# Performance work log

Hardware: AMD Instinct MI355X
Metric: run time of the kernel (lower is better)

Reference implementation:

```python
import jax, jax.numpy as jnp
import numpy as np
from jax import lax

STRIDE = 16
SCALES = (8.0, 16.0, 32.0)
RATIOS = (0.5, 1.0, 2.0)
PRE_NMS = 6000
POST_NMS = 300
NMS_THRESH = 0.7
MIN_SIZE = 16.0
DN = ('NCHW', 'OIHW', 'NCHW')


def _base_anchors():
    # 9 base anchors centered at (STRIDE/2, STRIDE/2), (ymin,xmin,ymax,xmax)
    c = STRIDE / 2.0
    rows = []
    for r in RATIOS:
        for s in SCALES:
            h = STRIDE * s * np.sqrt(r)
            w = STRIDE * s * np.sqrt(1.0 / r)
            rows.append([c - h / 2, c - w / 2, c + h / 2, c + w / 2])
    return jnp.asarray(np.array(rows, np.float32))


def _all_anchors(wdim, hdim):
    # shift base anchors over the (w, h) feature grid, matching permute(0,2,3,1) flatten order
    sy = jnp.arange(wdim, dtype=jnp.float32) * STRIDE
    sx = jnp.arange(hdim, dtype=jnp.float32) * STRIDE
    yy, xx = jnp.meshgrid(sy, sx, indexing='ij')
    shifts = jnp.stack([yy, xx, yy, xx], axis=-1).reshape(-1, 4)  # [w*h, 4]
    return (shifts[:, None, :] + _base_anchors()[None, :, :]).reshape(-1, 4)  # [w*h*9, 4]


def _conv(x, W, b, pad):
    y = lax.conv_general_dilated(x, W, (1, 1), pad, dimension_numbers=DN)
    return y + b[None, :, None, None]


def _nms_fixed(boxes, keep):
    # sequential greedy NMS over score-sorted boxes; returns POST_NMS boxes (zero padded)
    y1, x1, y2, x2 = boxes[:, 0], boxes[:, 1], boxes[:, 2], boxes[:, 3]
    areas = (y2 - y1) * (x2 - x1)
    N = boxes.shape[0]
    idxs = jnp.arange(N)

    def body(i, keep):
        yy1 = jnp.maximum(y1[i], y1)
        xx1 = jnp.maximum(x1[i], x1)
        yy2 = jnp.minimum(y2[i], y2)
        xx2 = jnp.minimum(x2[i], x2)
        inter = jnp.maximum(yy2 - yy1, 0.0) * jnp.maximum(xx2 - xx1, 0.0)
        iou = inter / (areas[i] + areas - inter + 1e-12)
        suppress = (iou > NMS_THRESH) & (idxs > i) & keep[i]
        return keep & ~suppress

    keep = lax.fori_loop(0, N, body, keep)
    rank = jnp.cumsum(keep) - 1
    slot = jnp.where(keep & (rank < POST_NMS), rank, POST_NMS)  # overflow slot
    out = jnp.zeros((POST_NMS + 1, 4), boxes.dtype).at[slot].set(boxes)
    return out[:POST_NMS]


def _proposals(loc, score_fg, anchors, img_h, img_w):
    ah = anchors[:, 2] - anchors[:, 0]
    aw = anchors[:, 3] - anchors[:, 1]
    acy = anchors[:, 0] + 0.5 * ah
    acx = anchors[:, 1] + 0.5 * aw
    cy = loc[:, 0] * ah + acy
    cx = loc[:, 1] * aw + acx
    h = jnp.exp(loc[:, 2]) * ah
    w = jnp.exp(loc[:, 3]) * aw
    boxes = jnp.stack([cy - 0.5 * h, cx - 0.5 * w, cy + 0.5 * h, cx + 0.5 * w], axis=-1)
    hi = jnp.array([img_h, img_w, img_h, img_w], dtype=boxes.dtype)
    boxes = jnp.clip(boxes, 0.0, hi)
    hs = boxes[:, 2] - boxes[:, 0]
    ws = boxes[:, 3] - boxes[:, 1]
    valid = (hs >= MIN_SIZE) & (ws >= MIN_SIZE)
    sc = jnp.where(valid, score_fg, -jnp.inf)
    top_sc, top_idx = lax.top_k(sc, PRE_NMS)
    cand = boxes[top_idx]
    return _nms_fixed(cand, jnp.isfinite(top_sc))


def setup_inputs() -> dict:
    key = jax.random.key(0)
    k = jax.random.split(key, 4)
    return {
        'base_feature_map': jax.random.normal(k[0], (8, 512, 50, 50), jnp.float32),
        'W_conv': jax.random.normal(k[1], (512, 512, 3, 3), jnp.float32) * 0.01,
        'b_conv': jnp.zeros((512,), jnp.float32),
        'W_cls': jax.random.normal(k[2], (18, 512, 1, 1), jnp.float32) * 0.01,
        'b_cls': jnp.zeros((18,), jnp.float32),
        'W_reg': jax.random.normal(k[3], (36, 512, 1, 1), jnp.float32) * 0.01,
        'b_reg': jnp.zeros((36,), jnp.float32),
        'img_h': 800,
        'img_w': 800,
    }


def reference(base_feature_map, W_conv, b_conv, W_cls, b_cls, W_reg, b_reg, img_h, img_w):
    n, _, w, h = base_feature_map.shape
    anchors = _all_anchors(w, h)  # [w*h*9, 4]
    x = jax.nn.relu(_conv(base_feature_map, W_conv, b_conv, 'SAME'))
    rpn_locs = _conv(x, W_reg, b_reg, 'VALID').transpose(0, 2, 3, 1).reshape(n, -1, 4)
    rpn_scores = _conv(x, W_cls, b_cls, 'VALID').transpose(0, 2, 3, 1).reshape(n, -1, 2)
    fg = jax.nn.softmax(rpn_scores[0], axis=-1)[:, 1]
    rois = _proposals(rpn_locs[0], fg, anchors, float(img_h), float(img_w))
    return rpn_locs, rpn_scores, anchors, rois
```

## Files before the change

### kernel.cpp

```cpp
#include <hip/hip_runtime.h>
#include <cstdint>
#include <math.h>

typedef unsigned int u32;
typedef unsigned long long u64;
typedef __attribute__((ext_vector_type(8))) short short8v;
typedef __attribute__((ext_vector_type(4))) float f32x4;

#define N_BATCH 8
#define C_IN    512
#define PX      2500
#define KDIM    4608
#define NA      22500
#define PRE_NMS 6000
#define POST_NMS 300

#define OUT_SCORES 720000
#define OUT_ANCH   1080000
#define OUT_ROIS   1170000

#define WS_X     0
#define WS_SCORE 10240000
#define WS_BOX   10262500
#define WS_LIST  10352500
#define WS_META  10388500
#define WS_WP    10388608
#define WS_XP    12747904
#define WS_END   22987904

#define NW_ELEMS (512 * KDIM)
#define NX_ELEMS (N_BATCH * C_IN * PX)

__device__ inline u32 rne_hi16(float f) {
    u32 u = __float_as_uint(f);
    return (u + 0x7FFFu + ((u >> 16) & 1u)) >> 16;
}
__device__ inline u32 pack_split(float f) {
    u32 rh  = rne_hi16(f);
    float d = f - __uint_as_float(rh << 16);
    u32 rl  = rne_hi16(d);
    return (rh << 16) | rl;
}

__global__ __launch_bounds__(256) void k_prep(const float* __restrict__ Wc,
                                              const float* __restrict__ in,
                                              u32* __restrict__ WP,
                                              u32* __restrict__ XP) {
    int o = blockIdx.x * 256 + threadIdx.x;
    if (o < NW_ELEMS) {
        int ci_in = o & 31;
        int tmp   = o >> 5;
        int r     = tmp % 9;
        int cc    = tmp / 9;
        int co    = cc >> 4;
        int cig   = cc & 15;
        int ci    = cig * 32 + ci_in;
        WP[o] = pack_split(Wc[(size_t)co * KDIM + ci * 9 + r]);
    } else {
        int o2 = o - NW_ELEMS;
        if (o2 < NX_ELEMS && XP) XP[o2] = pack_split(in[o2]);
    }
}

__global__ __launch_bounds__(256) void k_conv3(const float* __restrict__ in,
                                               const u32* __restrict__ XP,
                                               const u32* __restrict__ WP,
                                               const float* __restrict__ bc,
                                               float* __restrict__ xout) {
    __shared__ u32 Ap[128][32];
    __shared__ u32 Bp[128][32];

    int b  = blockIdx.x;
    int n  = b & 7;
    int q  = b >> 3;
    int cb = q & 3;
    int pt = q >> 2;
    int t  = threadIdx.x;
    int lane = t & 63;
    int w  = t >> 6;
    int wr = w >> 1, wc = w & 1;
    int px0 = pt * 128, co0 = cb * 128;
    const float* inN = in + (size_t)n * C_IN * PX;
    const u32*   XPn = XP ? (XP + (size_t)n * C_IN * PX) : nullptr;

    int sco = t >> 1;
    int skb = (t & 1) << 4;
    int spx = t & 127;
    int skk = (t >> 7) << 4;
    int gpx = px0 + spx;
    int sy  = gpx / 50;
    int sx  = gpx - sy * 50;
    bool pxok = (gpx < PX);
    const u32* wpA = WP + (size_t)(co0 + sco) * KDIM + skb;

    f32x4 acc[4][4];
#pragma unroll
    for (int i = 0; i < 4; ++i)
#pragma unroll
        for (int j = 0; j < 4; ++j) acc[i][j] = (f32x4)0.f;

    const int ro  = lane & 15;
    const int g8s = (lane >> 4) << 1;

    for (int cig = 0; cig < 16; ++cig) {
        int ci0 = cig << 5;
        for (int r = 0; r < 9; ++r) {
            int kstep = cig * 9 + r;
            {
                const u32* wp = wpA + kstep * 32;
                int rs = sco & 7;
#pragma unroll
                for (int qq = 0; qq < 4; ++qq) {
                    uint4 wv = *(const uint4*)(wp + qq * 4);
                    int slot = ((skb >> 2) + qq) ^ rs;
                    *(uint4*)&Ap[sco][slot << 2] = wv;
                }
            }
            {
                int ry = (r * 11) >> 5;
                int dy = ry - 1;
                int dx = r - ry * 3 - 1;
                int iy = sy + dy, ix = sx + dx;
                bool valid = pxok && ((unsigned)iy < 50u) && ((unsigned)ix < 50u);
                int off = iy * 50 + ix;
                u32 uu[16];
                if (XPn) {
                    const u32* bp = XPn + (size_t)(ci0 + skk) * PX + off;
#pragma unroll
                    for (int it = 0; it < 16; ++it)
                        uu[it] = valid ? bp[it * PX] : 0u;
                } else {
                    const float* bp = inN + (size_t)(ci0 + skk) * PX + off;
#pragma unroll
                    for (int it = 0; it < 16; ++it)
                        uu[it] = valid ? pack_split(bp[it * PX]) : 0u;
                }
                int rs = spx & 7;
#pragma unroll
                for (int qq = 0; qq < 4; ++qq) {
                    int slot = ((skk >> 2) + qq) ^ rs;
                    *(uint4*)&Bp[spx][slot << 2] = *(uint4*)&uu[qq * 4];
                }
            }
            __syncthreads();

            short8v aH[4], aL[4], bH[4], bL[4];
#pragma unroll
            for (int s = 0; s < 4; ++s) {
                {
                    int ra = wr * 64 + s * 16 + ro;
                    int rs = ra & 7;
                    u32 pa[8];
                    *(uint4*)&pa[0] = *(const uint4*)&Ap[ra][(g8s ^ rs) << 2];
                    *(uint4*)&pa[4] = *(const uint4*)&Ap[ra][((g8s + 1) ^ rs) << 2];
                    u32 h[4], l[4];
#pragma unroll
                    for (int w2 = 0; w2 < 4; ++w2) {
                        h[w2] = __builtin_amdgcn_perm(pa[2 * w2 + 1], pa[2 * w2], 0x07060302u);
                        l[w2] = __builtin_amdgcn_perm(pa[2 * w2 + 1], pa[2 * w2], 0x05040100u);
                    }
                    aH[s] = *(short8v*)h;
                    aL[s] = *(short8v*)l;
                }
                {
                    int rb = wc * 64 + s * 16 + ro;
                    int rs = rb & 7;
                    u32 pb[8];
                    *(uint4*)&pb[0] = *(const uint4*)&Bp[rb][(g8s ^ rs) << 2];
                    *(uint4*)&pb[4] = *(const uint4*)&Bp[rb][((g8s + 1) ^ rs) << 2];
                    u32 h[4], l[4];
#pragma unroll
                    for (int w2 = 0; w2 < 4; ++w2) {
                        h[w2] = __builtin_amdgcn_perm(pb[2 * w2 + 1], pb[2 * w2], 0x07060302u);
                        l[w2] = __builtin_amdgcn_perm(pb[2 * w2 + 1], pb[2 * w2], 0x05040100u);
                    }
                    bH[s] = *(short8v*)h;
                    bL[s] = *(short8v*)l;
                }
            }
#pragma unroll
            for (int i = 0; i < 4; ++i)
#pragma unroll
                for (int j = 0; j < 4; ++j) {
                    acc[i][j] = __builtin_amdgcn_mfma_f32_16x16x32_bf16(aH[i], bH[j], acc[i][j], 0, 0, 0);
                    acc[i][j] = __builtin_amdgcn_mfma_f32_16x16x32_bf16(aH[i], bL[j], acc[i][j], 0, 0, 0);
                    acc[i][j] = __builtin_amdgcn_mfma_f32_16x16x32_bf16(aL[i], bH[j], acc[i][j], 0, 0, 0);
                }
            __syncthreads();
        }
    }

    int coB  = co0 + wr * 64;
    int pxB  = px0 + wc * 64 + ro;
    int rowg = (lane >> 4) << 2;
#pragma unroll
    for (int i = 0; i < 4; ++i) {
#pragma unroll
        for (int rg = 0; rg < 4; ++rg) {
            int co = coB + i * 16 + rowg + rg;
            float bias = bc[co];
            float* dst = xout + ((size_t)n * C_IN + co) * PX;
#pragma unroll
            for (int j = 0; j < 4; ++j) {
                int px = pxB + j * 16;
                if (px < PX) dst[px] = fmaxf(acc[i][j][rg] + bias, 0.f);
            }
        }
    }
}

__device__ inline float readDim(const void* p) {
    int v = *(const int*)p;
    if (v > 0 && v <= 100000) return (float)v;
    return *(const float*)p;
}

__global__ __launch_bounds__(256) void k_heads(const float* __restrict__ x,
                                               const float* __restrict__ Wreg,
                                               const float* __restrict__ breg,
                                               const float* __restrict__ Wcls,
                                               const float* __restrict__ bcls,
                                               float* __restrict__ out,
                                               float* __restrict__ wsScore,
                                               float* __restrict__ wsBox,
                                               const void* pih, const void* piw) {
    __shared__ float As[32][68];
    __shared__ float Bs[32][132];
    __shared__ float Hs[54][132];
    int b  = blockIdx.x;
    int pt = b % 20, n = b / 20;
    int t  = threadIdx.x;
    int tx = t & 15, ty = t >> 4;
    int px0 = pt * 128;
    float acc[4][8];
#pragma unroll
    for (int i = 0; i < 4; ++i)
#pragma unroll
        for (int j = 0; j < 8; ++j) acc[i][j] = 0.f;

    for (int k0 = 0; k0 < 512; k0 += 32) {
        {
            int c   = t >> 2;
            int kkb = (t & 3) << 3;
            const float* src = nullptr;
            if (c < 36)      src = Wreg + (size_t)c * 512 + k0 + kkb;
            else if (c < 54) src = Wcls + (size_t)(c - 36) * 512 + k0 + kkb;
#pragma unroll
            for (int qq = 0; qq < 2; ++qq) {
                float4 wv = src ? *(const float4*)(src + qq * 4) : make_float4(0, 0, 0, 0);
                As[kkb + qq * 4 + 0][c] = wv.x;
                As[kkb + qq * 4 + 1][c] = wv.y;
                As[kkb + qq * 4 + 2][c] = wv.z;
                As[kkb + qq * 4 + 3][c] = wv.w;
            }
        }
        {
            int pxl = t & 127;
            int kk0 = (t >> 7) << 4;
            int px  = px0 + pxl;
#pragma unroll
            for (int it = 0; it < 16; ++it) {
                int kk = kk0 + it;
                float v = 0.f;
                if (px < PX) v = x[((size_t)n * 512 + k0 + kk) * PX + px];
                Bs[kk][pxl] = v;
            }
        }
        __syncthreads();
#pragma unroll 8
        for (int kk = 0; kk < 32; ++kk) {
            float a[4], bb[8];
            *(float4*)&a[0]  = *(const float4*)&As[kk][ty * 4];
            *(float4*)&bb[0] = *(const float4*)&Bs[kk][tx * 8];
            *(float4*)&bb[4] = *(const float4*)&Bs[kk][tx * 8 + 4];
#pragma unroll
            for (int i = 0; i < 4; ++i)
#pragma unroll
                for (int j = 0; j < 8; ++j)
                    acc[i][j] = fmaf(a[i], bb[j], acc[i][j]);
        }
        __syncthreads();
    }
    int pxb = px0 + tx * 8;
#pragma unroll
    for (int i = 0; i < 4; ++i) {
        int c = ty * 4 + i;
        if (c >= 54) continue;
        float bias = (c < 36) ? breg[c] : bcls[c - 36];
        for (int j = 0; j < 8; ++j) {
            int px = pxb + j;
            if (px >= PX) break;
            float v = acc[i][j] + bias;
            if (c < 36)
                out[(size_t)n * 90000 + (size_t)px * 36 + c] = v;
            else
                out[OUT_SCORES + (size_t)n * 45000 + (size_t)px * 18 + (c - 36)] = v;
            if (n == 0) Hs[c][tx * 8 + j] = v;
        }
    }

    if (n == 0) {
        __syncthreads();
        float imgH = readDim(pih), imgW = readDim(piw);
        const float ratios[3] = {0.5f, 1.f, 2.f};
        const float scales[3] = {8.f, 16.f, 32.f};
        for (int idx = t; idx < 128 * 9; idx += 256) {
            int pxl = idx / 9;
            int a   = idx - pxl * 9;
            int px  = px0 + pxl;
            if (px >= PX) continue;
            int gi = px * 9 + a;
            int y = px / 50, xq = px - y * 50;
            float r = ratios[a / 3], s = scales[a % 3];
            float hh = 16.f * s * sqrtf(r);
            float wv = 16.f * s * sqrtf(1.f / r);
            float ay1 = y * 16.f + 8.f - 0.5f * hh;
            float ax1 = xq * 16.f + 8.f - 0.5f * wv;
            float ay2 = y * 16.f + 8.f + 0.5f * hh;
            float ax2 = xq * 16.f + 8.f + 0.5f * wv;
            *(float4*)(out + OUT_ANCH + (size_t)gi * 4) = make_float4(ay1, ax1, ay2, ax2);

            float l0 = Hs[a * 4 + 0][pxl];
            float l1 = Hs[a * 4 + 1][pxl];
            float l2 = Hs[a * 4 + 2][pxl];
            float l3 = Hs[a * 4 + 3][pxl];
            float s0 = Hs[36 + 2 * a][pxl];
            float s1 = Hs[37 + 2 * a][pxl];
            float fg = 1.f / (1.f + expf(s0 - s1));
            float ah = ay2 - ay1, aw = ax2 - ax1;
            float acy = ay1 + 0.5f * ah, acx = ax1 + 0.5f * aw;
            float cy = l0 * ah + acy;
            float cx = l1 * aw + acx;
            float bh = expf(l2) * ah;
            float bw = expf(l3) * aw;
            float b0 = cy - 0.5f * bh, b1 = cx - 0.5f * bw;
            float b2 = cy + 0.5f * bh, b3 = cx + 0.5f * bw;
            b0 = fminf(fmaxf(b0, 0.f), imgH);
            b1 = fminf(fmaxf(b1, 0.f), imgW);
            b2 = fminf(fmaxf(b2, 0.f), imgH);
            b3 = fminf(fmaxf(b3, 0.f), imgW);
            bool valid = ((b2 - b0) >= 16.f) && ((b3 - b1) >= 16.f);
            wsScore[gi] = valid ? fg : -INFINITY;
            *(float4*)(wsBox + (size_t)gi * 4) = make_float4(b0, b1, b2, b3);
        }
    }
}

__device__ inline u32 fkey(float s) {
    u32 u = __float_as_uint(s);
    return (u & 0x80000000u) ? ~u : (u | 0x80000000u);
}

__global__ __launch_bounds__(1024) void k_select(const float* __restrict__ score,
                                                 u64* __restrict__ list,
                                                 int* __restrict__ meta) {
    __shared__ u32 hist[4096];
    __shared__ int sB1, sB2, sM3, sNeed, sV;
    __shared__ u32 sT32;
    __shared__ int cHi, cTie;
    int t = threadIdx.x;
    const int NT = 1024;

    for (int i = t; i < 4096; i += NT) hist[i] = 0;
    __syncthreads();
    for (int i = t; i < NA; i += NT) atomicAdd(&hist[fkey(score[i]) >> 20], 1u);
    __syncthreads();
    for (int off = 1; off < 4096; off <<= 1) {
        u32 v[4]; int c = 0;
        for (int bb = t; bb < 4096; bb += NT) { v[c++] = hist[bb] + ((bb + off < 4096) ? hist[bb + off] : 0u); }
        __syncthreads();
        c = 0;
        for (int bb = t; bb < 4096; bb += NT) hist[bb] = v[c++];
        __syncthreads();
    }
    for (int bb = t; bb < 4096; bb += NT) {
        u32 Sb  = hist[bb];
        u32 Sb1 = (bb < 4095) ? hist[bb + 1] : 0u;
        if (Sb >= PRE_NMS && Sb1 < PRE_NMS) sB1 = bb;
    }
    if (t == 0) sV = (int)hist[2048];
    __syncthreads();
    int B1 = sB1;
    int m1 = (B1 < 4095) ? (int)hist[B1 + 1] : 0;
    int V  = sV;
    __syncthreads();

    for (int i = t; i < 4096; i += NT) hist[i] = 0;
    __syncthreads();
    for (int i = t; i < NA; i += NT) {
        u32 key = fkey(score[i]);
        if ((int)(key >> 20) == B1) atomicAdd(&hist[(key >> 8) & 0xFFFu], 1u);
    }
    __syncthreads();
    for (int off = 1; off < 4096; off <<= 1) {
        u32 v[4]; int c = 0;
        for (int bb = t; bb < 4096; bb += NT) { v[c++] = hist[bb] + ((bb + off < 4096) ? hist[bb + off] : 0u); }
        __syncthreads();
        c = 0;
        for (int bb = t; bb < 4096; bb += NT) hist[bb] = v[c++];
        __syncthreads();
    }
    for (int bb = t; bb < 4096; bb += NT) {
        int Sb  = m1 + (int)hist[bb];
        int Sb1 = m1 + (int)((bb < 4095) ? hist[bb + 1] : 0u);
        if (Sb >= PRE_NMS && Sb1 < PRE_NMS) sB2 = bb;
    }
    __syncthreads();
    int B2 = sB2;
    int m2 = m1 + (int)((B2 < 4095) ? hist[B2 + 1] : 0u);
    u32 P24 = ((u32)B1 << 12) | (u32)B2;
    __syncthreads();

    for (int i = t; i < 256; i += NT) hist[i] = 0;
    __syncthreads();
    for (int i = t; i < NA; i += NT) {
        u32 key = fkey(score[i]);
        if ((key >> 8) == P24) atomicAdd(&hist[key & 0xFFu], 1u);
    }
    __syncthreads();
    for (int off = 1; off < 256; off <<= 1) {
        u32 v[1]; int c = 0;
        for (int bb = t; bb < 256; bb += NT) { v[c++] = hist[bb] + ((bb + off < 256) ? hist[bb + off] : 0u); }
        __syncthreads();
        c = 0;
        for (int bb = t; bb < 256; bb += NT) hist[bb] = v[c++];
        __syncthreads();
    }
    for (int bb = t; bb < 256; bb += NT) {
        int Sb  = m2 + (int)hist[bb];
        int Sb1 = m2 + (int)((bb < 255) ? hist[bb + 1] : 0u);
        if (Sb >= PRE_NMS && Sb1 < PRE_NMS) {
            sM3   = m2 + (int)((bb < 255) ? hist[bb + 1] : 0u);
            sNeed = PRE_NMS - sM3;
            sT32  = (P24 << 8) | (u32)bb;
        }
    }
    if (t == 0) { cHi = 0; cTie = 0; meta[0] = (V < PRE_NMS) ? V : PRE_NMS; }
    __syncthreads();
    int m3 = sM3, need = sNeed;
    u32 T32 = sT32;

    for (int i = t; i < NA; i += NT) {
        u32 key = fkey(score[i]);
        u64 comp = ((u64)key << 32) | (u64)(0xFFFFFFFFu - (u32)i);
        if (key > T32) {
            int p = atomicAdd(&cHi, 1);
            list[p] = comp;
        } else if (key == T32) {
            int p = atomicAdd(&cTie, 1);
            if (p < need) list[m3 + p] = comp;
        }
    }
    for (int i = PRE_NMS + t; i < 8192; i += NT) list[i] = 0ull;
}

__global__ __launch_bounds__(1024) void k_presort(u64* __restrict__ list) {
    __shared__ u64 ls[1024];
    int t  = threadIdx.x;
    int gi = (blockIdx.x << 10) + t;
    ls[t] = list[gi];
    __syncthreads();
    for (int k = 2; k <= 1024; k <<= 1) {
        for (int j = k >> 1; j > 0; j >>= 1) {
            int ixj = t ^ j;
            if (ixj > t) {
                u64 a = ls[t], b = ls[ixj];
                bool desc = ((gi & k) == 0);
                if (desc ? (a < b) : (a > b)) { ls[t] = b; ls[ixj] = a; }
            }
            __syncthreads();
        }
    }
    list[gi] = ls[t];
}

__global__ __launch_bounds__(1024) void k_mergenms(const u64* __restrict__ list,
                                                   const float* __restrict__ boxes,
                                                   const int* __restrict__ meta,
                                                   float* __restrict__ rois) {
    __shared__ u64 sb[8192];
    __shared__ float kb[POST_NMS][4];
    __shared__ float cb4[64][4];
    __shared__ u32 KLo[64], KHi[64], supA[64];
    __shared__ int sKept;
    int t = threadIdx.x;
    const int NT = 1024;

    for (int i = t; i < 8192; i += NT) sb[i] = list[i];
    __syncthreads();

    for (int k = 2048; k <= 8192; k <<= 1) {
        for (int j = k >> 1; j > 0; j >>= 1) {
            for (int i = t; i < 8192; i += NT) {
                int ixj = i ^ j;
                if (ixj > i) {
                    u64 a = sb[i], bv = sb[ixj];
                    bool desc = ((i & k) == 0);
                    if (desc ? (a < bv) : (a > bv)) { sb[i] = bv; sb[ixj] = a; }
                }
            }
            __syncthreads();
        }
    }

    int keepN = meta[0];
    if (t == 0) sKept = 0;
    __syncthreads();

    int s = t >> 4, g = t & 15;
    for (int c0 = 0; c0 < PRE_NMS; c0 += 64) {
        if (sKept >= POST_NMS) break;
        if (t < 64) {
            u32 bidx = 0xFFFFFFFFu - (u32)sb[c0 + t];
            if (bidx >= NA) bidx = 0;
            float4 bx = *(const float4*)(boxes + (size_t)bidx * 4);
            cb4[t][0] = bx.x; cb4[t][1] = bx.y; cb4[t][2] = bx.z; cb4[t][3] = bx.w;
            KLo[t] = 0; KHi[t] = 0; supA[t] = 0;
        }
        __syncthreads();

        float y1 = cb4[s][0], x1 = cb4[s][1], y2 = cb4[s][2], x2 = cb4[s][3];
        float area = (y2 - y1) * (x2 - x1);

        u32 klo = 0, khi = 0;
#pragma unroll
        for (int qq = 0; qq < 4; ++qq) {
            int j = g * 4 + qq;
            if (j > s) {
                float jy1 = cb4[j][0], jx1 = cb4[j][1], jy2 = cb4[j][2], jx2 = cb4[j][3];
                float yy1 = fmaxf(y1, jy1), xx1 = fmaxf(x1, jx1);
                float yy2 = fminf(y2, jy2), xx2 = fminf(x2, jx2);
                float inter = fmaxf(yy2 - yy1, 0.f) * fmaxf(xx2 - xx1, 0.f);
                float ja = (jy2 - jy1) * (jx2 - jx1);
                float iou = inter / (area + ja - inter + 1e-12f);
                if (iou > 0.7f) { if (j < 32) klo |= 1u << j; else khi |= 1u << (j - 32); }
            }
        }
        if (klo) atomicOr(&KLo[s], klo);
        if (khi) atomicOr(&KHi[s], khi);

        int kept0 = sKept;
        bool supf = false;
        for (int jj = g; jj < kept0; jj += 16) {
            float ky1 = kb[jj][0], kx1 = kb[jj][1], ky2 = kb[jj][2], kx2 = kb[jj][3];
            float yy1 = fmaxf(ky1, y1), xx1 = fmaxf(kx1, x1);
            float yy2 = fminf(ky2, y2), xx2 = fminf(kx2, x2);
            float inter = fmaxf(yy2 - yy1, 0.f) * fmaxf(xx2 - xx1, 0.f);
            float karea = (ky2 - ky1) * (kx2 - kx1);
            float iou = inter / (karea + area - inter + 1e-12f);
            if (iou > 0.7f) { supf = true; break; }
        }
        if (supf) atomicOr(&supA[s], 1u);
        __syncthreads();

        if (t == 0) {
            u64 supm = 0;
            int kept = sKept;
            for (int s2 = 0; s2 < 64 && kept < POST_NMS; ++s2) {
                if (c0 + s2 >= keepN) continue;
                if (supA[s2]) continue;
                if ((supm >> s2) & 1ull) continue;
                kb[kept][0] = cb4[s2][0]; kb[kept][1] = cb4[s2][1];
                kb[kept][2] = cb4[s2][2]; kb[kept][3] = cb4[s2][3];
                *(float4*)(rois + (size_t)kept * 4) =
                    make_float4(cb4[s2][0], cb4[s2][1], cb4[s2][2], cb4[s2][3]);
                kept++;
                supm |= ((u64)KHi[s2] << 32) | (u64)KLo[s2];
            }
            sKept = kept;
        }
        __syncthreads();
    }

    int kf = sKept;
    for (int r = kf * 4 + t; r < POST_NMS * 4; r += NT) rois[r] = 0.f;
}

extern "C" void kernel_launch(void* const* d_in, const int* in_sizes, int n_in,
                              void* d_out, int out_size, void* d_ws, size_t ws_size,
                              hipStream_t stream) {
    const float* feat = (const float*)d_in[0];
    const float* Wc   = (const float*)d_in[1];
    const float* bc   = (const float*)d_in[2];
    const float* Wcls = (const float*)d_in[3];
    const float* bcls = (const float*)d_in[4];
    const float* Wreg = (const float*)d_in[5];
    const float* breg = (const float*)d_in[6];
    const void* pih   = d_in[7];
    const void* piw   = d_in[8];
    float* out = (float*)d_out;
    float* ws  = (float*)d_ws;

    u32* WP   = (u32*)(ws + WS_WP);
    u64* list = (u64*)(ws + WS_LIST);
    int* meta = (int*)(ws + WS_META);
    bool haveXP = (ws_size >= (size_t)WS_END * sizeof(float));
    u32* XP = haveXP ? (u32*)(ws + WS_XP) : nullptr;

    int prepItems = NW_ELEMS + (haveXP ? NX_ELEMS : 0);
    hipLaunchKernelGGL(k_prep, dim3((prepItems + 255) / 256), dim3(256), 0, stream, Wc, feat, WP, XP);
    hipLaunchKernelGGL(k_conv3, dim3(640), dim3(256), 0, stream, feat, XP, WP, bc, ws + WS_X);
    hipLaunchKernelGGL(k_heads, dim3(160), dim3(256), 0, stream, ws + WS_X, Wreg, breg, Wcls, bcls,
                       out, ws + WS_SCORE, ws + WS_BOX, pih, piw);
    hipLaunchKernelGGL(k_select, dim3(1), dim3(1024), 0, stream, ws + WS_SCORE, list, meta);
    hipLaunchKernelGGL(k_presort, dim3(8), dim3(1024), 0, stream, list);
    hipLaunchKernelGGL(k_mergenms, dim3(1), dim3(1024), 0, stream, list, ws + WS_BOX, meta, out + OUT_ROIS);
}
```

Measured before the change: 639.5 us.

## Rebalance heads tiling, presort 2048-element runs, and widen NMS chunk to 128

The 1x1 head GEMM now uses 64-pixel tiles with 2x8 register blocking, doubling the grid to 320 blocks to fill more CUs. The presort kernel sorts 2048-element runs in 4 blocks, so the single-block merge starts at k=4096 and does fewer bitonic stages. Greedy NMS now processes 128 candidates per iteration with 128-bit suppression masks, halving the number of serial iterations and barriers. In exchange, each heads block reloads the weights more often and the serial thread-0 scan covers more candidates per step.

```diff
diff --git a/kernel.cpp b/kernel.cpp
--- a/kernel.cpp
+++ b/kernel.cpp
@@ -225,16 +225,16 @@
                                                float* __restrict__ wsBox,
                                                const void* pih, const void* piw) {
     __shared__ float As[32][68];
-    __shared__ float Bs[32][132];
-    __shared__ float Hs[54][132];
+    __shared__ float Bs[32][68];
+    __shared__ float Hs[54][64];
     int b  = blockIdx.x;
-    int pt = b % 20, n = b / 20;
+    int pt = b % 40, n = b / 40;
     int t  = threadIdx.x;
-    int tx = t & 15, ty = t >> 4;
-    int px0 = pt * 128;
-    float acc[4][8];
-#pragma unroll
-    for (int i = 0; i < 4; ++i)
+    int tx = t & 7, ty = t >> 3;
+    int px0 = pt * 64;
+    float acc[2][8];
+#pragma unroll
+    for (int i = 0; i < 2; ++i)
 #pragma unroll
         for (int j = 0; j < 8; ++j) acc[i][j] = 0.f;
 
@@ -255,11 +255,11 @@
             }
         }
         {
-            int pxl = t & 127;
-            int kk0 = (t >> 7) << 4;
+            int pxl = t & 63;
+            int kk0 = (t >> 6) << 3;
             int px  = px0 + pxl;
 #pragma unroll
-            for (int it = 0; it < 16; ++it) {
+            for (int it = 0; it < 8; ++it) {
                 int kk = kk0 + it;
                 float v = 0.f;
                 if (px < PX) v = x[((size_t)n * 512 + k0 + kk) * PX + px];
@@ -269,22 +269,22 @@
         __syncthreads();
 #pragma unroll 8
         for (int kk = 0; kk < 32; ++kk) {
-            float a[4], bb[8];
-            *(float4*)&a[0]  = *(const float4*)&As[kk][ty * 4];
+            float a0 = As[kk][ty * 2], a1 = As[kk][ty * 2 + 1];
+            float bb[8];
             *(float4*)&bb[0] = *(const float4*)&Bs[kk][tx * 8];
             *(float4*)&bb[4] = *(const float4*)&Bs[kk][tx * 8 + 4];
 #pragma unroll
-            for (int i = 0; i < 4; ++i)
-#pragma unroll
-                for (int j = 0; j < 8; ++j)
-                    acc[i][j] = fmaf(a[i], bb[j], acc[i][j]);
+            for (int j = 0; j < 8; ++j) {
+                acc[0][j] = fmaf(a0, bb[j], acc[0][j]);
+                acc[1][j] = fmaf(a1, bb[j], acc[1][j]);
+            }
         }
         __syncthreads();
     }
     int pxb = px0 + tx * 8;
 #pragma unroll
-    for (int i = 0; i < 4; ++i) {
-        int c = ty * 4 + i;
+    for (int i = 0; i < 2; ++i) {
+        int c = ty * 2 + i;
         if (c >= 54) continue;
         float bias = (c < 36) ? breg[c] : bcls[c - 36];
         for (int j = 0; j < 8; ++j) {
@@ -304,7 +304,7 @@
         float imgH = readDim(pih), imgW = readDim(piw);
         const float ratios[3] = {0.5f, 1.f, 2.f};
         const float scales[3] = {8.f, 16.f, 32.f};
-        for (int idx = t; idx < 128 * 9; idx += 256) {
+        for (int idx = t; idx < 64 * 9; idx += 256) {
             int pxl = idx / 9;
             int a   = idx - pxl * 9;
             int px  = px0 + pxl;
@@ -455,23 +455,27 @@
 }
 
 __global__ __launch_bounds__(1024) void k_presort(u64* __restrict__ list) {
-    __shared__ u64 ls[1024];
-    int t  = threadIdx.x;
-    int gi = (blockIdx.x << 10) + t;
-    ls[t] = list[gi];
-    __syncthreads();
-    for (int k = 2; k <= 1024; k <<= 1) {
+    __shared__ u64 ls[2048];
+    int t    = threadIdx.x;
+    int base = blockIdx.x << 11;
+    ls[t] = list[base + t];
+    ls[t + 1024] = list[base + t + 1024];
+    __syncthreads();
+    for (int k = 2; k <= 2048; k <<= 1) {
         for (int j = k >> 1; j > 0; j >>= 1) {
-            int ixj = t ^ j;
-            if (ixj > t) {
-                u64 a = ls[t], b = ls[ixj];
-                bool desc = ((gi & k) == 0);
-                if (desc ? (a < b) : (a > b)) { ls[t] = b; ls[ixj] = a; }
+            for (int i = t; i < 2048; i += 1024) {
+                int ixj = i ^ j;
+                if (ixj > i) {
+                    u64 a = ls[i], b2 = ls[ixj];
+                    bool desc = (((base + i) & k) == 0);
+                    if (desc ? (a < b2) : (a > b2)) { ls[i] = b2; ls[ixj] = a; }
+                }
             }
             __syncthreads();
         }
     }
-    list[gi] = ls[t];
+    list[base + t] = ls[t];
+    list[base + t + 1024] = ls[t + 1024];
 }
 
 __global__ __launch_bounds__(1024) void k_mergenms(const u64* __restrict__ list,
@@ -480,8 +484,9 @@
                                                    float* __restrict__ rois) {
     __shared__ u64 sb[8192];
     __shared__ float kb[POST_NMS][4];
-    __shared__ float cb4[64][4];
-    __shared__ u32 KLo[64], KHi[64], supA[64];
+    __shared__ float cb4[128][4];
+    __shared__ u32 Kw[128][4];
+    __shared__ u32 supA[128];
     __shared__ int sKept;
     int t = threadIdx.x;
     const int NT = 1024;
@@ -489,7 +494,7 @@
     for (int i = t; i < 8192; i += NT) sb[i] = list[i];
     __syncthreads();
 
-    for (int k = 2048; k <= 8192; k <<= 1) {
+    for (int k = 4096; k <= 8192; k <<= 1) {
         for (int j = k >> 1; j > 0; j >>= 1) {
             for (int i = t; i < 8192; i += NT) {
                 int ixj = i ^ j;
@@ -507,25 +512,26 @@
     if (t == 0) sKept = 0;
     __syncthreads();
 
-    int s = t >> 4, g = t & 15;
-    for (int c0 = 0; c0 < PRE_NMS; c0 += 64) {
+    int s = t >> 3, g = t & 7;
+    for (int c0 = 0; c0 < PRE_NMS; c0 += 128) {
         if (sKept >= POST_NMS) break;
-        if (t < 64) {
+        if (t < 128) {
             u32 bidx = 0xFFFFFFFFu - (u32)sb[c0 + t];
             if (bidx >= NA) bidx = 0;
             float4 bx = *(const float4*)(boxes + (size_t)bidx * 4);
             cb4[t][0] = bx.x; cb4[t][1] = bx.y; cb4[t][2] = bx.z; cb4[t][3] = bx.w;
-            KLo[t] = 0; KHi[t] = 0; supA[t] = 0;
+            Kw[t][0] = 0; Kw[t][1] = 0; Kw[t][2] = 0; Kw[t][3] = 0;
+            supA[t] = 0;
         }
         __syncthreads();
 
         float y1 = cb4[s][0], x1 = cb4[s][1], y2 = cb4[s][2], x2 = cb4[s][3];
         float area = (y2 - y1) * (x2 - x1);
 
-        u32 klo = 0, khi = 0;
-#pragma unroll
-        for (int qq = 0; qq < 4; ++qq) {
-            int j = g * 4 + qq;
+        u32 kbits = 0;
+#pragma unroll
+        for (int qq = 0; qq < 16; ++qq) {
+            int j = g * 16 + qq;
             if (j > s) {
                 float jy1 = cb4[j][0], jx1 = cb4[j][1], jy2 = cb4[j][2], jx2 = cb4[j][3];
                 float yy1 = fmaxf(y1, jy1), xx1 = fmaxf(x1, jx1);
@@ -533,15 +539,14 @@
                 float inter = fmaxf(yy2 - yy1, 0.f) * fmaxf(xx2 - xx1, 0.f);
                 float ja = (jy2 - jy1) * (jx2 - jx1);
                 float iou = inter / (area + ja - inter + 1e-12f);
-                if (iou > 0.7f) { if (j < 32) klo |= 1u << j; else khi |= 1u << (j - 32); }
-            }
-        }
-        if (klo) atomicOr(&KLo[s], klo);
-        if (khi) atomicOr(&KHi[s], khi);
+                if (iou > 0.7f) kbits |= 1u << (j & 31);
+            }
+        }
+        if (kbits) atomicOr(&Kw[s][g >> 1], kbits);
 
         int kept0 = sKept;
         bool supf = false;
-        for (int jj = g; jj < kept0; jj += 16) {
+        for (int jj = g; jj < kept0; jj += 8) {
             float ky1 = kb[jj][0], kx1 = kb[jj][1], ky2 = kb[jj][2], kx2 = kb[jj][3];
             float yy1 = fmaxf(ky1, y1), xx1 = fmaxf(kx1, x1);
             float yy2 = fminf(ky2, y2), xx2 = fminf(kx2, x2);
@@ -554,18 +559,20 @@
         __syncthreads();
 
         if (t == 0) {
-            u64 supm = 0;
+            u64 m0 = 0, m1 = 0;
             int kept = sKept;
-            for (int s2 = 0; s2 < 64 && kept < POST_NMS; ++s2) {
+            for (int s2 = 0; s2 < 128 && kept < POST_NMS; ++s2) {
                 if (c0 + s2 >= keepN) continue;
                 if (supA[s2]) continue;
-                if ((supm >> s2) & 1ull) continue;
+                bool supm = (s2 < 64) ? ((m0 >> s2) & 1ull) : ((m1 >> (s2 - 64)) & 1ull);
+                if (supm) continue;
                 kb[kept][0] = cb4[s2][0]; kb[kept][1] = cb4[s2][1];
                 kb[kept][2] = cb4[s2][2]; kb[kept][3] = cb4[s2][3];
                 *(float4*)(rois + (size_t)kept * 4) =
                     make_float4(cb4[s2][0], cb4[s2][1], cb4[s2][2], cb4[s2][3]);
                 kept++;
-                supm |= ((u64)KHi[s2] << 32) | (u64)KLo[s2];
+                m0 |= ((u64)Kw[s2][1] << 32) | (u64)Kw[s2][0];
+                m1 |= ((u64)Kw[s2][3] << 32) | (u64)Kw[s2][2];
             }
             sKept = kept;
         }
@@ -600,9 +607,9 @@
     int prepItems = NW_ELEMS + (haveXP ? NX_ELEMS : 0);
     hipLaunchKernelGGL(k_prep, dim3((prepItems + 255) / 256), dim3(256), 0, stream, Wc, feat, WP, XP);
     hipLaunchKernelGGL(k_conv3, dim3(640), dim3(256), 0, stream, feat, XP, WP, bc, ws + WS_X);
-    hipLaunchKernelGGL(k_heads, dim3(160), dim3(256), 0, stream, ws + WS_X, Wreg, breg, Wcls, bcls,
+    hipLaunchKernelGGL(k_heads, dim3(320), dim3(256), 0, stream, ws + WS_X, Wreg, breg, Wcls, bcls,
                        out, ws + WS_SCORE, ws + WS_BOX, pih, piw);
     hipLaunchKernelGGL(k_select, dim3(1), dim3(1024), 0, stream, ws + WS_SCORE, list, meta);
-    hipLaunchKernelGGL(k_presort, dim3(8), dim3(1024), 0, stream, list);
+    hipLaunchKernelGGL(k_presort, dim3(4), dim3(1024), 0, stream, list);
     hipLaunchKernelGGL(k_mergenms, dim3(1), dim3(1024), 0, stream, list, ws + WS_BOX, meta, out + OUT_ROIS);
 }
```

New measurement: 617.2 us (median of 3 runs). 3.5% less time.
